# Performance work log

Hardware: AMD Instinct MI355X
Metric: run time of the kernel (lower is better)

## Reference

```python
import jax, jax.numpy as jnp
import numpy as np

N_USER = 1_000_000
N_ITEM = 100_000
E = 16          # embedding_size
O = 16          # out_size per head
H = 4           # head_num
HID = 32        # hidden_size
B = 8192        # batch
S = 200         # sample_num
L = 50          # history length
NSUPP = 50_000  # supp_user_num


def _xavier(key, shape):
    fan_in, fan_out = shape[-2], shape[-1]
    std = np.sqrt(2.0 / (fan_in + fan_out))
    return (jax.random.normal(key, shape) * std).astype(jnp.float32)


def setup_inputs() -> dict:
    key = jax.random.key(0)
    ks = jax.random.split(key, 16)
    uid = jax.random.randint(ks[0], (B,), 0, N_USER)
    iid = jax.random.randint(ks[1], (B,), 0, N_ITEM)
    return {
        "user_embedding": _xavier(ks[2], (N_USER, E)),
        "item_embedding": _xavier(ks[3], (N_ITEM, E)),
        "wq": _xavier(ks[4], (H, E, O)),   # per-head Wq (no bias)
        "wk": _xavier(ks[5], (H, E, O)),
        "wv": _xavier(ks[6], (H, O, O)),
        "w_out": _xavier(ks[7], (H * O, O)),
        "l1_w": _xavier(ks[8], (3 * E, HID)),
        "l1_b": jnp.full((HID,), 0.1, jnp.float32),
        "l2_w": _xavier(ks[9], (HID, HID // 2)),
        "l2_b": jnp.full((HID // 2,), 0.1, jnp.float32),
        "l3_w": _xavier(ks[10], (HID // 2, 1)),
        "l3_b": jnp.full((1,), 0.1, jnp.float32),
        "user_bias": jnp.zeros((N_USER, 1), jnp.float32),
        "item_bias": jnp.zeros((N_ITEM, 1), jnp.float32),
        "x": jnp.stack([uid, iid], axis=1),                          # [B,2]
        "history": jax.random.randint(ks[11], (B, L), 0, N_ITEM),    # [B,L]
        "history_len": jax.random.randint(ks[12], (B,), 1, L + 1),   # [B] >=1
        "supp_users": jax.random.randint(ks[13], (NSUPP,), 0, N_USER),
        "sample_index": jax.random.randint(ks[14], (H, B, S), 0, NSUPP),
    }


def reference(user_embedding, item_embedding, wq, wk, wv, w_out,
              l1_w, l1_b, l2_w, l2_b, l3_w, l3_b, user_bias, item_bias,
              x, history, history_len, supp_users, sample_index):
    user_id = x[:, 0]
    item_id = x[:, 1]

    # user init embedding = mean-by-len of full (unmasked) history, as in source
    hist_emb = item_embedding[history]                                # [B,L,E]
    user_init = hist_emb.sum(axis=1) / history_len[:, None].astype(jnp.float32)  # [B,E]

    # per-head GAT over sampled support users (all heads vectorized)
    nb = user_embedding[supp_users[sample_index]]                     # [H,B,S,E]
    q = jnp.einsum('be,heo->hbo', user_init, wq)                      # [H,B,O]
    k = jnp.einsum('hbse,heo->hbso', nb, wk)                          # [H,B,S,O]
    attn = jax.nn.softmax(jnp.einsum('hbo,hbso->hbs', q, k), axis=-1)
    ctx = jnp.einsum('hbs,hbso->hbo', attn, k)                        # [H,B,O]
    gat = jnp.einsum('hbo,hop->hbp', ctx, wv)                         # [H,B,O]
    gat = jnp.transpose(gat, (1, 0, 2)).reshape(B, H * O)             # concat heads

    user_emb = gat @ w_out                                            # [B,O]
    item_emb = item_embedding[item_id]                                # [B,E]
    interaction = user_emb * item_emb
    ratings = interaction.sum(axis=1)

    h = jnp.concatenate([user_emb, item_emb, interaction], axis=1)    # [B,3E]
    x1 = jnp.tanh(h @ l1_w + l1_b)
    x2 = jnp.tanh(x1 @ l2_w + l2_b)
    x3 = (x2 @ l3_w + l3_b).reshape(-1)

    ub = user_bias[user_id, 0]
    ib = item_bias[item_id, 0]
    return (ratings + x3) / 2.0 + ub + ib
```

## Files before the change

kernel.cpp:

```cpp
#include <hip/hip_runtime.h>
#include <math.h>

#define N_USERS 1000000
#define N_ITEMS 100000
#define EMB 16
#define OUTD 16
#define NH 4
#define HID 32
#define BB 8192
#define SS 200
#define LL 50
#define NSUPP 50000

typedef float v4f __attribute__((ext_vector_type(4)));

__global__ __launch_bounds__(256) void k_supp_kernel(
    const float* __restrict__ user_emb,
    const int*   __restrict__ supp_users,
    const float* __restrict__ wk,
    float*       __restrict__ Ksupp)
{
    __shared__ float s_wk[NH * EMB * OUTD];
    __shared__ float s_u[16][EMB];
    int t = threadIdx.x;
    for (int i = t; i < NH * EMB * OUTD; i += 256) s_wk[i] = wk[i];
    int n0 = blockIdx.x * 16;
    {
        int ul = t >> 4, e = t & 15;
        int row = supp_users[n0 + ul];
        s_u[ul][e] = user_emb[(size_t)row * EMB + e];
    }
    __syncthreads();
    int h   = t >> 6;
    int sub = (t >> 4) & 3;
    int o   = t & 15;
#pragma unroll
    for (int r = 0; r < 4; ++r) {
        int ul = sub + 4 * r;
        float acc = 0.f;
#pragma unroll
        for (int e = 0; e < EMB; ++e)
            acc += s_u[ul][e] * s_wk[(h * EMB + e) * OUTD + o];
        Ksupp[((size_t)h * NSUPP + n0 + ul) * OUTD + o] = acc;
    }
}

__global__ __launch_bounds__(256) void user_init_q_kernel(
    const float* __restrict__ item_emb,
    const int*   __restrict__ history,
    const int*   __restrict__ history_len,
    const float* __restrict__ wq,
    float*       __restrict__ qbuf)
{
    __shared__ float s_ui[4][EMB];
    __shared__ float s_wq[NH * EMB * OUTD];
    int t = threadIdx.x;
    for (int i = t; i < NH * EMB * OUTD; i += 256) s_wq[i] = wq[i];

    int g    = t >> 6;
    int lane = t & 63;
    int l4   = lane >> 4;
    int e    = lane & 15;
    int b    = blockIdx.x * 4 + g;

    float sum = 0.f;
    for (int l = l4; l < LL; l += 4) {
        int it = __builtin_nontemporal_load(history + (size_t)b * LL + l);
        sum += item_emb[(size_t)it * EMB + e];
    }
    sum += __shfl_xor(sum, 16);
    sum += __shfl_xor(sum, 32);
    if (lane < EMB) s_ui[g][lane] = sum / (float)history_len[b];
    __syncthreads();

    int h  = (t >> 4) & 3;
    int o  = t & 15;
    float acc = 0.f;
#pragma unroll
    for (int ee = 0; ee < EMB; ++ee)
        acc += s_ui[g][ee] * s_wq[(h * EMB + ee) * OUTD + o];
    qbuf[((size_t)b * NH + h) * OUTD + o] = acc;
}

__global__ __launch_bounds__(256, 4) void attn_kernel(
    const float* __restrict__ Ksupp,
    const float* __restrict__ qbuf,
    const int*   __restrict__ sample_index,
    const float* __restrict__ wv,
    float*       __restrict__ gat)
{
    int blk   = blockIdx.x;
    int h     = (blk & 7) >> 1;
    int btile = ((blk >> 3) << 1) | (blk & 1);
    int wave  = threadIdx.x >> 6;
    int lane  = threadIdx.x & 63;
    int b     = btile * 4 + wave;
    int g     = lane >> 2;
    int qt    = lane & 3;

    const int* si = sample_index + ((size_t)h * BB + b) * SS;
    int pre0 = __builtin_nontemporal_load(si + lane);
    int pre1 = __builtin_nontemporal_load(si + lane + 64);
    int pre2 = __builtin_nontemporal_load(si + lane + 128);
    int pre3 = (lane < 8) ? __builtin_nontemporal_load(si + lane + 192) : 0;

    v4f qv = __builtin_nontemporal_load(
        (const v4f*)(qbuf + ((size_t)b * NH + h) * OUTD) + qt);

    const float* Kh = Ksupp + (size_t)h * NSUPP * OUTD;

    int idx[13];
#pragma unroll
    for (int r = 0; r < 13; ++r) {
        int pre = (r < 4) ? pre0 : (r < 8) ? pre1 : (r < 12) ? pre2 : pre3;
        idx[r] = __shfl(pre, (r & 3) * 16 + g, 64);
    }

    v4f kq[13];
#pragma unroll
    for (int r = 0; r < 13; ++r)
        kq[r] = *(const v4f*)(Kh + (size_t)idx[r] * OUTD + qt * 4);

    float d[13];
#pragma unroll
    for (int r = 0; r < 13; ++r) {
        float p = kq[r].x * qv.x + kq[r].y * qv.y + kq[r].z * qv.z + kq[r].w * qv.w;
        p += __shfl_xor(p, 1);
        p += __shfl_xor(p, 2);
        d[r] = p;
    }
    if (g >= 8) d[12] = -3.0e38f;

    float m = d[0];
#pragma unroll
    for (int r = 1; r < 13; ++r) m = fmaxf(m, d[r]);
#pragma unroll
    for (int off = 4; off < 64; off <<= 1) m = fmaxf(m, __shfl_xor(m, off));

    float l = 0.f;
    v4f c = {0.f, 0.f, 0.f, 0.f};
#pragma unroll
    for (int r = 0; r < 13; ++r) {
        float w = __expf(d[r] - m);
        l += w;
        c += w * kq[r];
    }
#pragma unroll
    for (int off = 4; off < 64; off <<= 1) {
        l   += __shfl_xor(l, off);
        c.x += __shfl_xor(c.x, off);
        c.y += __shfl_xor(c.y, off);
        c.z += __shfl_xor(c.z, off);
        c.w += __shfl_xor(c.w, off);
    }
    float inv = 1.f / l;

    float part = c.x * wv[((size_t)h * OUTD + qt * 4 + 0) * OUTD + g]
               + c.y * wv[((size_t)h * OUTD + qt * 4 + 1) * OUTD + g]
               + c.z * wv[((size_t)h * OUTD + qt * 4 + 2) * OUTD + g]
               + c.w * wv[((size_t)h * OUTD + qt * 4 + 3) * OUTD + g];
    part += __shfl_xor(part, 1);
    part += __shfl_xor(part, 2);
    if (qt == 0)
        gat[(size_t)b * (NH * OUTD) + h * OUTD + g] = part * inv;
}

__global__ __launch_bounds__(256) void epilogue_kernel(
    const float* __restrict__ gat,
    const float* __restrict__ item_emb,
    const float* __restrict__ w_out,
    const float* __restrict__ l1_w, const float* __restrict__ l1_b,
    const float* __restrict__ l2_w, const float* __restrict__ l2_b,
    const float* __restrict__ l3_w, const float* __restrict__ l3_b,
    const float* __restrict__ user_bias, const float* __restrict__ item_bias,
    const int*   __restrict__ x,
    float*       __restrict__ out)
{
    int t    = threadIdx.x;
    int g    = t >> 6;
    int lane = t & 63;
    int b    = blockIdx.x * 4 + g;

    __shared__ float s_gat[4][NH * OUTD];
    __shared__ float s_ue[4][OUTD];
    __shared__ float s_ie[4][EMB];
    __shared__ float s_x1[4][HID];
    __shared__ float s_x2[4][HID / 2];

    int uid = x[(size_t)b * 2 + 0];
    int iid = x[(size_t)b * 2 + 1];

    s_gat[g][lane] = gat[(size_t)b * (NH * OUTD) + lane];
    if (lane < EMB) s_ie[g][lane] = item_emb[(size_t)iid * EMB + lane];
    __syncthreads();

    if (lane < OUTD) {
        float acc = 0.f;
#pragma unroll
        for (int j = 0; j < NH * OUTD; ++j) acc += s_gat[g][j] * w_out[j * OUTD + lane];
        s_ue[g][lane] = acc;
    }
    __syncthreads();

    if (lane < HID) {
        float acc = l1_b[lane];
#pragma unroll
        for (int i = 0; i < EMB; ++i) {
            float ue = s_ue[g][i], ie = s_ie[g][i];
            acc += ue * l1_w[i * HID + lane]
                 + ie * l1_w[(EMB + i) * HID + lane]
                 + ue * ie * l1_w[(2 * EMB + i) * HID + lane];
        }
        s_x1[g][lane] = tanhf(acc);
    }
    __syncthreads();

    if (lane < HID / 2) {
        float acc = l2_b[lane];
#pragma unroll
        for (int j = 0; j < HID; ++j) acc += s_x1[g][j] * l2_w[j * (HID / 2) + lane];
        s_x2[g][lane] = tanhf(acc);
    }
    __syncthreads();

    if (lane == 0) {
        float x3 = l3_b[0];
#pragma unroll
        for (int j = 0; j < HID / 2; ++j) x3 += s_x2[g][j] * l3_w[j];
        float ratings = 0.f;
#pragma unroll
        for (int o = 0; o < OUTD; ++o) ratings += s_ue[g][o] * s_ie[g][o];
        out[b] = 0.5f * (ratings + x3) + user_bias[uid] + item_bias[iid];
    }
}

extern "C" void kernel_launch(void* const* d_in, const int* in_sizes, int n_in,
                              void* d_out, int out_size, void* d_ws, size_t ws_size,
                              hipStream_t stream) {
    const float* user_embedding = (const float*)d_in[0];
    const float* item_embedding = (const float*)d_in[1];
    const float* wq             = (const float*)d_in[2];
    const float* wk             = (const float*)d_in[3];
    const float* wv             = (const float*)d_in[4];
    const float* w_out          = (const float*)d_in[5];
    const float* l1_w           = (const float*)d_in[6];
    const float* l1_b           = (const float*)d_in[7];
    const float* l2_w           = (const float*)d_in[8];
    const float* l2_b           = (const float*)d_in[9];
    const float* l3_w           = (const float*)d_in[10];
    const float* l3_b           = (const float*)d_in[11];
    const float* user_bias      = (const float*)d_in[12];
    const float* item_bias      = (const float*)d_in[13];
    const int*   x              = (const int*)d_in[14];
    const int*   history        = (const int*)d_in[15];
    const int*   history_len    = (const int*)d_in[16];
    const int*   supp_users     = (const int*)d_in[17];
    const int*   sample_index   = (const int*)d_in[18];
    float* out = (float*)d_out;

    char* ws = (char*)d_ws;
    float* Ksupp = (float*)ws;
    ws += (size_t)NH * NSUPP * OUTD * sizeof(float);
    float* qbuf  = (float*)ws;
    ws += (size_t)BB * NH * OUTD * sizeof(float);
    float* gat   = (float*)ws;

    k_supp_kernel<<<NSUPP / 16, 256, 0, stream>>>(user_embedding, supp_users, wk, Ksupp);
    user_init_q_kernel<<<BB / 4, 256, 0, stream>>>(item_embedding, history, history_len, wq, qbuf);
    attn_kernel<<<NH * BB / 4, 256, 0, stream>>>(Ksupp, qbuf, sample_index, wv, gat);
    epilogue_kernel<<<BB / 4, 256, 0, stream>>>(
        gat, item_embedding, w_out, l1_w, l1_b, l2_w, l2_b, l3_w, l3_b,
        user_bias, item_bias, x, out);
}
```

Before: 213.3 us.

## Store projected keys in fp16 and fuse kernels into prep and attention-epilogue

Merges the key-projection and query kernels into one launch split by block index, and fuses the attention and MLP epilogue into one kernel with one block per batch row and one wave per head. The projected support-user keys are stored as fp16, which halves the bytes of the random gathers in attention. This removes two launches and the gat buffer round trip through global memory. The cost is lower precision of the keys and an epilogue in which only one wave of each block does useful work.

```diff
diff --git a/kernel.cpp b/kernel.cpp
--- a/kernel.cpp
+++ b/kernel.cpp
@@ -13,160 +13,79 @@
 #define NSUPP 50000
 
 typedef float v4f __attribute__((ext_vector_type(4)));
-
-__global__ __launch_bounds__(256) void k_supp_kernel(
+typedef _Float16 h4 __attribute__((ext_vector_type(4)));
+
+__global__ __launch_bounds__(256) void prep_kernel(
     const float* __restrict__ user_emb,
     const int*   __restrict__ supp_users,
     const float* __restrict__ wk,
-    float*       __restrict__ Ksupp)
-{
-    __shared__ float s_wk[NH * EMB * OUTD];
-    __shared__ float s_u[16][EMB];
-    int t = threadIdx.x;
-    for (int i = t; i < NH * EMB * OUTD; i += 256) s_wk[i] = wk[i];
-    int n0 = blockIdx.x * 16;
-    {
-        int ul = t >> 4, e = t & 15;
-        int row = supp_users[n0 + ul];
-        s_u[ul][e] = user_emb[(size_t)row * EMB + e];
-    }
-    __syncthreads();
-    int h   = t >> 6;
-    int sub = (t >> 4) & 3;
-    int o   = t & 15;
-#pragma unroll
-    for (int r = 0; r < 4; ++r) {
-        int ul = sub + 4 * r;
-        float acc = 0.f;
-#pragma unroll
-        for (int e = 0; e < EMB; ++e)
-            acc += s_u[ul][e] * s_wk[(h * EMB + e) * OUTD + o];
-        Ksupp[((size_t)h * NSUPP + n0 + ul) * OUTD + o] = acc;
-    }
-}
-
-__global__ __launch_bounds__(256) void user_init_q_kernel(
+    _Float16*    __restrict__ Ksupp,
     const float* __restrict__ item_emb,
     const int*   __restrict__ history,
     const int*   __restrict__ history_len,
     const float* __restrict__ wq,
     float*       __restrict__ qbuf)
 {
+    __shared__ float s_wk[NH * EMB * OUTD];
+    __shared__ float s_u[16][EMB];
     __shared__ float s_ui[4][EMB];
     __shared__ float s_wq[NH * EMB * OUTD];
+
     int t = threadIdx.x;
-    for (int i = t; i < NH * EMB * OUTD; i += 256) s_wq[i] = wq[i];
-
-    int g    = t >> 6;
-    int lane = t & 63;
-    int l4   = lane >> 4;
-    int e    = lane & 15;
-    int b    = blockIdx.x * 4 + g;
-
-    float sum = 0.f;
-    for (int l = l4; l < LL; l += 4) {
-        int it = __builtin_nontemporal_load(history + (size_t)b * LL + l);
-        sum += item_emb[(size_t)it * EMB + e];
-    }
-    sum += __shfl_xor(sum, 16);
-    sum += __shfl_xor(sum, 32);
-    if (lane < EMB) s_ui[g][lane] = sum / (float)history_len[b];
-    __syncthreads();
-
-    int h  = (t >> 4) & 3;
-    int o  = t & 15;
-    float acc = 0.f;
-#pragma unroll
-    for (int ee = 0; ee < EMB; ++ee)
-        acc += s_ui[g][ee] * s_wq[(h * EMB + ee) * OUTD + o];
-    qbuf[((size_t)b * NH + h) * OUTD + o] = acc;
+    if (blockIdx.x < NSUPP / 16) {
+        for (int i = t; i < NH * EMB * OUTD; i += 256) s_wk[i] = wk[i];
+        int n0 = blockIdx.x * 16;
+        {
+            int ul = t >> 4, e = t & 15;
+            int row = supp_users[n0 + ul];
+            s_u[ul][e] = user_emb[(size_t)row * EMB + e];
+        }
+        __syncthreads();
+        int h   = t >> 6;
+        int sub = (t >> 4) & 3;
+        int o   = t & 15;
+#pragma unroll
+        for (int r = 0; r < 4; ++r) {
+            int ul = sub + 4 * r;
+            float acc = 0.f;
+#pragma unroll
+            for (int e = 0; e < EMB; ++e)
+                acc += s_u[ul][e] * s_wk[(h * EMB + e) * OUTD + o];
+            Ksupp[((size_t)h * NSUPP + n0 + ul) * OUTD + o] = (_Float16)acc;
+        }
+    } else {
+        for (int i = t; i < NH * EMB * OUTD; i += 256) s_wq[i] = wq[i];
+        int g    = t >> 6;
+        int lane = t & 63;
+        int l4   = lane >> 4;
+        int e    = lane & 15;
+        int b    = (blockIdx.x - NSUPP / 16) * 4 + g;
+
+        float sum = 0.f;
+        for (int l = l4; l < LL; l += 4) {
+            int it = __builtin_nontemporal_load(history + (size_t)b * LL + l);
+            sum += item_emb[(size_t)it * EMB + e];
+        }
+        sum += __shfl_xor(sum, 16);
+        sum += __shfl_xor(sum, 32);
+        if (lane < EMB) s_ui[g][lane] = sum / (float)history_len[b];
+        __syncthreads();
+
+        int h = (t >> 4) & 3;
+        int o = t & 15;
+        float acc = 0.f;
+#pragma unroll
+        for (int ee = 0; ee < EMB; ++ee)
+            acc += s_ui[g][ee] * s_wq[(h * EMB + ee) * OUTD + o];
+        qbuf[((size_t)b * NH + h) * OUTD + o] = acc;
+    }
 }
 
-__global__ __launch_bounds__(256, 4) void attn_kernel(
-    const float* __restrict__ Ksupp,
+__global__ __launch_bounds__(256, 4) void attn_epi_kernel(
+    const _Float16* __restrict__ Ksupp,
     const float* __restrict__ qbuf,
     const int*   __restrict__ sample_index,
     const float* __restrict__ wv,
-    float*       __restrict__ gat)
-{
-    int blk   = blockIdx.x;
-    int h     = (blk & 7) >> 1;
-    int btile = ((blk >> 3) << 1) | (blk & 1);
-    int wave  = threadIdx.x >> 6;
-    int lane  = threadIdx.x & 63;
-    int b     = btile * 4 + wave;
-    int g     = lane >> 2;
-    int qt    = lane & 3;
-
-    const int* si = sample_index + ((size_t)h * BB + b) * SS;
-    int pre0 = __builtin_nontemporal_load(si + lane);
-    int pre1 = __builtin_nontemporal_load(si + lane + 64);
-    int pre2 = __builtin_nontemporal_load(si + lane + 128);
-    int pre3 = (lane < 8) ? __builtin_nontemporal_load(si + lane + 192) : 0;
-
-    v4f qv = __builtin_nontemporal_load(
-        (const v4f*)(qbuf + ((size_t)b * NH + h) * OUTD) + qt);
-
-    const float* Kh = Ksupp + (size_t)h * NSUPP * OUTD;
-
-    int idx[13];
-#pragma unroll
-    for (int r = 0; r < 13; ++r) {
-        int pre = (r < 4) ? pre0 : (r < 8) ? pre1 : (r < 12) ? pre2 : pre3;
-        idx[r] = __shfl(pre, (r & 3) * 16 + g, 64);
-    }
-
-    v4f kq[13];
-#pragma unroll
-    for (int r = 0; r < 13; ++r)
-        kq[r] = *(const v4f*)(Kh + (size_t)idx[r] * OUTD + qt * 4);
-
-    float d[13];
-#pragma unroll
-    for (int r = 0; r < 13; ++r) {
-        float p = kq[r].x * qv.x + kq[r].y * qv.y + kq[r].z * qv.z + kq[r].w * qv.w;
-        p += __shfl_xor(p, 1);
-        p += __shfl_xor(p, 2);
-        d[r] = p;
-    }
-    if (g >= 8) d[12] = -3.0e38f;
-
-    float m = d[0];
-#pragma unroll
-    for (int r = 1; r < 13; ++r) m = fmaxf(m, d[r]);
-#pragma unroll
-    for (int off = 4; off < 64; off <<= 1) m = fmaxf(m, __shfl_xor(m, off));
-
-    float l = 0.f;
-    v4f c = {0.f, 0.f, 0.f, 0.f};
-#pragma unroll
-    for (int r = 0; r < 13; ++r) {
-        float w = __expf(d[r] - m);
-        l += w;
-        c += w * kq[r];
-    }
-#pragma unroll
-    for (int off = 4; off < 64; off <<= 1) {
-        l   += __shfl_xor(l, off);
-        c.x += __shfl_xor(c.x, off);
-        c.y += __shfl_xor(c.y, off);
-        c.z += __shfl_xor(c.z, off);
-        c.w += __shfl_xor(c.w, off);
-    }
-    float inv = 1.f / l;
-
-    float part = c.x * wv[((size_t)h * OUTD + qt * 4 + 0) * OUTD + g]
-               + c.y * wv[((size_t)h * OUTD + qt * 4 + 1) * OUTD + g]
-               + c.z * wv[((size_t)h * OUTD + qt * 4 + 2) * OUTD + g]
-               + c.w * wv[((size_t)h * OUTD + qt * 4 + 3) * OUTD + g];
-    part += __shfl_xor(part, 1);
-    part += __shfl_xor(part, 2);
-    if (qt == 0)
-        gat[(size_t)b * (NH * OUTD) + h * OUTD + g] = part * inv;
-}
-
-__global__ __launch_bounds__(256) void epilogue_kernel(
-    const float* __restrict__ gat,
     const float* __restrict__ item_emb,
     const float* __restrict__ w_out,
     const float* __restrict__ l1_w, const float* __restrict__ l1_b,
@@ -176,60 +95,129 @@
     const int*   __restrict__ x,
     float*       __restrict__ out)
 {
-    int t    = threadIdx.x;
-    int g    = t >> 6;
-    int lane = t & 63;
-    int b    = blockIdx.x * 4 + g;
-
-    __shared__ float s_gat[4][NH * OUTD];
-    __shared__ float s_ue[4][OUTD];
-    __shared__ float s_ie[4][EMB];
-    __shared__ float s_x1[4][HID];
-    __shared__ float s_x2[4][HID / 2];
+    int b    = blockIdx.x;
+    int h    = threadIdx.x >> 6;
+    int lane = threadIdx.x & 63;
+    int g    = lane >> 2;
+    int qt   = lane & 3;
+
+    __shared__ float s_gat[NH * OUTD];
+    __shared__ float s_ue[OUTD];
+    __shared__ float s_ie[EMB];
+    __shared__ float s_x1[HID];
+    __shared__ float s_x2[HID / 2];
+
+    const int* si = sample_index + ((size_t)h * BB + b) * SS;
+    int pre0 = __builtin_nontemporal_load(si + lane);
+    int pre1 = __builtin_nontemporal_load(si + lane + 64);
+    int pre2 = __builtin_nontemporal_load(si + lane + 128);
+    int pre3 = (lane < 8) ? __builtin_nontemporal_load(si + lane + 192) : 0;
+
+    v4f qv = __builtin_nontemporal_load(
+        (const v4f*)(qbuf + ((size_t)b * NH + h) * OUTD) + qt);
+
+    const h4* K4 = (const h4*)(Ksupp + (size_t)h * NSUPP * OUTD);
+
+    int idx[13];
+#pragma unroll
+    for (int r = 0; r < 13; ++r) {
+        int pre = (r < 4) ? pre0 : (r < 8) ? pre1 : (r < 12) ? pre2 : pre3;
+        idx[r] = __shfl(pre, (r & 3) * 16 + g, 64);
+    }
+
+    h4 kq[13];
+#pragma unroll
+    for (int r = 0; r < 13; ++r)
+        kq[r] = K4[(size_t)idx[r] * 4 + qt];
+
+    float d[13];
+#pragma unroll
+    for (int r = 0; r < 13; ++r) {
+        v4f kf = __builtin_convertvector(kq[r], v4f);
+        float p = kf.x * qv.x + kf.y * qv.y + kf.z * qv.z + kf.w * qv.w;
+        p += __shfl_xor(p, 1);
+        p += __shfl_xor(p, 2);
+        d[r] = p;
+    }
+    if (g >= 8) d[12] = -3.0e38f;
+
+    float m = d[0];
+#pragma unroll
+    for (int r = 1; r < 13; ++r) m = fmaxf(m, d[r]);
+#pragma unroll
+    for (int off = 4; off < 64; off <<= 1) m = fmaxf(m, __shfl_xor(m, off));
+
+    float l = 0.f;
+    v4f c = {0.f, 0.f, 0.f, 0.f};
+#pragma unroll
+    for (int r = 0; r < 13; ++r) {
+        float w = __expf(d[r] - m);
+        v4f kf = __builtin_convertvector(kq[r], v4f);
+        l += w;
+        c += w * kf;
+    }
+#pragma unroll
+    for (int off = 4; off < 64; off <<= 1) {
+        l   += __shfl_xor(l, off);
+        c.x += __shfl_xor(c.x, off);
+        c.y += __shfl_xor(c.y, off);
+        c.z += __shfl_xor(c.z, off);
+        c.w += __shfl_xor(c.w, off);
+    }
+    float inv = 1.f / l;
+
+    float part = c.x * wv[((size_t)h * OUTD + qt * 4 + 0) * OUTD + g]
+               + c.y * wv[((size_t)h * OUTD + qt * 4 + 1) * OUTD + g]
+               + c.z * wv[((size_t)h * OUTD + qt * 4 + 2) * OUTD + g]
+               + c.w * wv[((size_t)h * OUTD + qt * 4 + 3) * OUTD + g];
+    part += __shfl_xor(part, 1);
+    part += __shfl_xor(part, 2);
+    if (qt == 0)
+        s_gat[h * OUTD + g] = part * inv;
+    __syncthreads();
 
     int uid = x[(size_t)b * 2 + 0];
     int iid = x[(size_t)b * 2 + 1];
-
-    s_gat[g][lane] = gat[(size_t)b * (NH * OUTD) + lane];
-    if (lane < EMB) s_ie[g][lane] = item_emb[(size_t)iid * EMB + lane];
-    __syncthreads();
-
-    if (lane < OUTD) {
-        float acc = 0.f;
-#pragma unroll
-        for (int j = 0; j < NH * OUTD; ++j) acc += s_gat[g][j] * w_out[j * OUTD + lane];
-        s_ue[g][lane] = acc;
-    }
-    __syncthreads();
-
-    if (lane < HID) {
+    if (h == 0) {
+        if (lane < EMB) s_ie[lane] = item_emb[(size_t)iid * EMB + lane];
+        if (lane < OUTD) {
+            float acc = 0.f;
+#pragma unroll
+            for (int j = 0; j < NH * OUTD; ++j)
+                acc += s_gat[j] * w_out[j * OUTD + lane];
+            s_ue[lane] = acc;
+        }
+    }
+    __syncthreads();
+
+    if (h == 0 && lane < HID) {
         float acc = l1_b[lane];
 #pragma unroll
         for (int i = 0; i < EMB; ++i) {
-            float ue = s_ue[g][i], ie = s_ie[g][i];
+            float ue = s_ue[i], ie = s_ie[i];
             acc += ue * l1_w[i * HID + lane]
                  + ie * l1_w[(EMB + i) * HID + lane]
                  + ue * ie * l1_w[(2 * EMB + i) * HID + lane];
         }
-        s_x1[g][lane] = tanhf(acc);
-    }
-    __syncthreads();
-
-    if (lane < HID / 2) {
+        s_x1[lane] = tanhf(acc);
+    }
+    __syncthreads();
+
+    if (h == 0 && lane < HID / 2) {
         float acc = l2_b[lane];
 #pragma unroll
-        for (int j = 0; j < HID; ++j) acc += s_x1[g][j] * l2_w[j * (HID / 2) + lane];
-        s_x2[g][lane] = tanhf(acc);
-    }
-    __syncthreads();
-
-    if (lane == 0) {
+        for (int j = 0; j < HID; ++j) acc += s_x1[j] * l2_w[j * (HID / 2) + lane];
+        s_x2[lane] = tanhf(acc);
+    }
+    __syncthreads();
+
+    if (h == 0 && lane == 0) {
         float x3 = l3_b[0];
 #pragma unroll
-        for (int j = 0; j < HID / 2; ++j) x3 += s_x2[g][j] * l3_w[j];
+        for (int j = 0; j < HID / 2; ++j) x3 += s_x2[j] * l3_w[j];
         float ratings = 0.f;
 #pragma unroll
-        for (int o = 0; o < OUTD; ++o) ratings += s_ue[g][o] * s_ie[g][o];
+        for (int o = 0; o < OUTD; ++o) ratings += s_ue[o] * s_ie[o];
         out[b] = 0.5f * (ratings + x3) + user_bias[uid] + item_bias[iid];
     }
 }
@@ -259,16 +247,15 @@
     float* out = (float*)d_out;
 
     char* ws = (char*)d_ws;
-    float* Ksupp = (float*)ws;
-    ws += (size_t)NH * NSUPP * OUTD * sizeof(float);
+    _Float16* Ksupp = (_Float16*)ws;
+    ws += (size_t)NH * NSUPP * OUTD * sizeof(_Float16);
     float* qbuf  = (float*)ws;
-    ws += (size_t)BB * NH * OUTD * sizeof(float);
-    float* gat   = (float*)ws;
-
-    k_supp_kernel<<<NSUPP / 16, 256, 0, stream>>>(user_embedding, supp_users, wk, Ksupp);
-    user_init_q_kernel<<<BB / 4, 256, 0, stream>>>(item_embedding, history, history_len, wq, qbuf);
-    attn_kernel<<<NH * BB / 4, 256, 0, stream>>>(Ksupp, qbuf, sample_index, wv, gat);
-    epilogue_kernel<<<BB / 4, 256, 0, stream>>>(
-        gat, item_embedding, w_out, l1_w, l1_b, l2_w, l2_b, l3_w, l3_b,
+
+    prep_kernel<<<NSUPP / 16 + BB / 4, 256, 0, stream>>>(
+        user_embedding, supp_users, wk, Ksupp,
+        item_embedding, history, history_len, wq, qbuf);
+    attn_epi_kernel<<<BB, 256, 0, stream>>>(
+        Ksupp, qbuf, sample_index, wv, item_embedding, w_out,
+        l1_w, l1_b, l2_w, l2_b, l3_w, l3_b,
         user_bias, item_bias, x, out);
 }
```

Result: slower. 226.5 us (+6.2%).
